# Kernel optimization log

Hardware: AMD Instinct MI355X
Metric: run time of the kernel (lower is better)

## Reference

```python
import jax, jax.numpy as jnp
import numpy as np

N_NODES = 50000
N_EDGES = 800000
F_IN, HID, N_CLS = 128, 64, 40
KS = 2  # kernel_size, dim=1, open B-spline, degree=1


def spline_conv(x, src, dst, pseudo, W, root, bias, num_nodes, kernel_size):
    """SplineConv (torch_geometric), dim=1, degree=1, open spline, aggr='mean'."""
    K = kernel_size
    v = pseudo[:, 0] * (K - 1)                       # map [0,1] -> [0, K-1]
    k0 = jnp.clip(jnp.floor(v), 0, K - 2)
    frac = v - k0                                    # linear (degree-1) basis
    i0 = k0.astype(jnp.int32)
    i1 = i0 + 1
    E = src.shape[0]
    e = jnp.arange(E)
    # per-edge kernel coefficients c[e,k] = sum_s basis[e,s]*[idx[e,s]==k]
    c = jnp.zeros((E, K), x.dtype).at[e, i0].add(1.0 - frac).at[e, i1].add(frac)
    xj = x[src]                                      # [E, F_in] gather
    # agg[k] = scatter-add over edges of c[e,k]*xj[e] -> [K, N, F_in]
    agg = jnp.stack([
        jax.ops.segment_sum(c[:, k:k + 1] * xj, dst, num_segments=num_nodes)
        for k in range(K)
    ])
    deg = jax.ops.segment_sum(jnp.ones((E,), x.dtype), dst, num_segments=num_nodes)
    msg = jnp.einsum('kni,kio->no', agg, W) / jnp.maximum(deg, 1.0)[:, None]
    return msg + x @ root + bias


def setup_inputs() -> dict:
    key = jax.random.key(0)
    ks = jax.random.split(key, 9)
    def glorot(k, shape):
        fan_in, fan_out = shape[-2], shape[-1]
        lim = (6.0 / (fan_in + fan_out)) ** 0.5
        return jax.random.uniform(k, shape, jnp.float32, -lim, lim)
    return {
        'x': jax.random.normal(ks[0], (N_NODES, F_IN), jnp.float32),
        'edge_index': jax.random.randint(ks[1], (2, N_EDGES), 0, N_NODES, jnp.int32),
        'edge_attr': jax.random.uniform(ks[2], (N_EDGES, 1), jnp.float32),
        'W1': glorot(ks[3], (KS, F_IN, HID)),
        'root1': glorot(ks[4], (F_IN, HID)),
        'bias1': jnp.zeros((HID,), jnp.float32),
        'W2': glorot(ks[5], (KS, HID, N_CLS)),
        'root2': glorot(ks[6], (HID, N_CLS)),
        'bias2': jnp.zeros((N_CLS,), jnp.float32),
    }


def reference(x, edge_index, edge_attr, W1, root1, bias1, W2, root2, bias2):
    src, dst = edge_index[0], edge_index[1]
    # eval mode: dropout is identity
    h = spline_conv(x, src, dst, edge_attr, W1, root1, bias1, N_NODES, KS)
    h = jax.nn.elu(h)
    out = spline_conv(h, src, dst, edge_attr, W2, root2, bias2, N_NODES, KS)
    return out
```

## Files before the change

### kernel.cpp

```cpp
#include <hip/hip_runtime.h>
#include <math.h>

#define N_NODES 50000
#define N_EDGES 800000
#define F_IN    128
#define HID     64
#define N_CLS   40

#define M1 (3 * HID)
#define K2  192
#define C2P 64

#define RANGE_SZ 6250
#define PERM_SLICES 128
#define PERM_CHUNK (N_EDGES / PERM_SLICES)
#define EST 64

#define NW (M1 * F_IN + C2P * K2)

using sh8 = __attribute__((ext_vector_type(8))) short;
using floatx4 = __attribute__((ext_vector_type(4))) float;

__device__ inline unsigned short f2bf(float f) {
    union { float f; unsigned int u; } c{f};
    unsigned int r = (c.u + 0x7FFF + ((c.u >> 16) & 1)) >> 16;
    return (unsigned short)r;
}
__device__ inline float bf2f(unsigned int u) {
    union { unsigned int u; float f; } c;
    c.u = u << 16;
    return c.f;
}

__global__ void concat_w(const float* __restrict__ W1, const float* __restrict__ root1,
                         const float* __restrict__ W2, const float* __restrict__ root2,
                         unsigned short* __restrict__ WT1, unsigned short* __restrict__ WT2,
                         int* __restrict__ cnt) {
    int i = blockIdx.x * blockDim.x + threadIdx.x;
    if (i < M1 * F_IN) {
        int c = i / F_IN, k = i % F_IN;
        float val;
        if (c < HID)            val = W1[k * HID + c];
        else if (c < 2 * HID)   val = W1[F_IN * HID + k * HID + (c - HID)];
        else                    val = root1[k * HID + (c - 2 * HID)];
        WT1[i] = f2bf(val);
    } else if (i < NW) {
        int ii = i - M1 * F_IN;
        int c = ii / K2, k = ii % K2;
        float val = 0.0f;
        if (c < N_CLS) {
            if (k < HID)             val = W2[k * N_CLS + c];
            else if (k < 2 * HID)    val = W2[HID * N_CLS + (k - HID) * N_CLS + c];
            else                     val = root2[(k - 2 * HID) * N_CLS + c];
        }
        WT2[ii] = f2bf(val);
    } else {
        int ii = i - NW;
        if (ii < N_NODES) cnt[ii] = 0;
    }
}

template <int KD, bool AF32, int SPLIT, int PW, int ROOTW, int MT>
__device__ __forceinline__ void gemm_body(int bid, const void* __restrict__ Aptr,
                                          const unsigned short* __restrict__ Bt,
                                          unsigned short* __restrict__ Csp,
                                          float* __restrict__ Croot, int Crows) {
    constexpr int KP = KD + 8;
    __shared__ unsigned short As[64 * KP];
    __shared__ unsigned short Bs[64 * KP];

    int tid = threadIdx.x;
    int row0 = bid * 64;

    if (AF32) {
        const float* A = (const float*)Aptr;
        for (int c = tid; c < 64 * (KD / 4); c += 256) {
            int r = c / (KD / 4), q = c % (KD / 4);
            int gr = row0 + r;
            float4 v = make_float4(0.f, 0.f, 0.f, 0.f);
            if (gr < Crows) v = *(const float4*)(A + (size_t)gr * KD + q * 4);
            union { unsigned short s[4]; uint2 u; } pk;
            pk.s[0] = f2bf(v.x); pk.s[1] = f2bf(v.y);
            pk.s[2] = f2bf(v.z); pk.s[3] = f2bf(v.w);
            *(uint2*)&As[r * KP + q * 4] = pk.u;
        }
    } else {
        const unsigned short* A = (const unsigned short*)Aptr;
        for (int c = tid; c < 64 * (KD / 8); c += 256) {
            int r = c / (KD / 8), q = c % (KD / 8);
            int gr = row0 + r;
            sh8 v = {};
            if (gr < Crows) v = *(const sh8*)(A + (size_t)gr * KD + q * 8);
            *(sh8*)&As[r * KP + q * 8] = v;
        }
    }

    int wv = tid >> 6, lane = tid & 63;
    int lrow = lane & 15, lq = lane >> 4;

    for (int mt = 0; mt < MT; ++mt) {
        int c0 = mt * 64;
        __syncthreads();
        for (int c = tid; c < 64 * (KD / 8); c += 256) {
            int r = c / (KD / 8), q = c % (KD / 8);
            *(sh8*)&Bs[r * KP + q * 8] = *(const sh8*)(Bt + (size_t)(c0 + r) * KD + q * 8);
        }
        __syncthreads();

        floatx4 acc[4] = {{0.f,0.f,0.f,0.f},{0.f,0.f,0.f,0.f},{0.f,0.f,0.f,0.f},{0.f,0.f,0.f,0.f}};
#pragma unroll
        for (int kt = 0; kt < KD / 32; ++kt) {
            int kb = kt * 32 + lq * 8;
            sh8 a0 = *(const sh8*)&As[(wv * 16 + lrow) * KP + kb];
#pragma unroll
            for (int cf = 0; cf < 4; ++cf) {
                sh8 b = *(const sh8*)&Bs[(cf * 16 + lrow) * KP + kb];
                acc[cf] = __builtin_amdgcn_mfma_f32_16x16x32_bf16(a0, b, acc[cf], 0, 0, 0);
            }
        }

#pragma unroll
        for (int r = 0; r < 4; ++r) {
            int gr = row0 + wv * 16 + lq * 4 + r;
            if (gr >= Crows) continue;
#pragma unroll
            for (int cf = 0; cf < 4; ++cf) {
                int gc = c0 + cf * 16 + lrow;
                float val = acc[cf][r];
                if (gc < SPLIT) {
                    int pi = (gc < PW) ? gc * 2 : (gc - PW) * 2 + 1;
                    Csp[(size_t)gr * SPLIT + pi] = f2bf(val);
                } else if (gc < SPLIT + ROOTW) {
                    Croot[(size_t)gr * ROOTW + (gc - SPLIT)] = val;
                }
            }
        }
    }
}

__device__ __forceinline__ void permute_body(int b, const int* __restrict__ src,
                                             const int* __restrict__ dst,
                                             const float* __restrict__ attr,
                                             int* __restrict__ cnt,
                                             unsigned int* __restrict__ edata) {
    int range = b & 7;
    int slice = b >> 3;
    int lo = range * RANGE_SZ;
    int e0 = slice * PERM_CHUNK;
    int e1 = e0 + PERM_CHUNK;
    for (int e = e0 + (int)threadIdx.x; e < e1; e += 256) {
        int d = dst[e];
        if ((unsigned)(d - lo) < (unsigned)RANGE_SZ) {
            int pos = atomicAdd(&cnt[d], 1);
            if (pos < EST) {
                unsigned int q = (unsigned int)(attr[e] * 65535.0f + 0.5f);
                edata[d * EST + pos] = (unsigned int)src[e] | (q << 16);
            }
        }
    }
}

__global__ __launch_bounds__(256) void gemm1_permute(const float* __restrict__ x,
                                                     const unsigned short* __restrict__ WT1,
                                                     unsigned short* __restrict__ Ysp,
                                                     float* __restrict__ Yroot,
                                                     const int* __restrict__ src,
                                                     const int* __restrict__ dst,
                                                     const float* __restrict__ attr,
                                                     int* __restrict__ cnt,
                                                     unsigned int* __restrict__ edata,
                                                     int gemmBlocks) {
    if ((int)blockIdx.x < gemmBlocks) {
        gemm_body<128, true, 128, 64, 64, 3>(blockIdx.x, (const void*)x, WT1, Ysp, Yroot, N_NODES);
    } else {
        permute_body(blockIdx.x - gemmBlocks, src, dst, attr, cnt, edata);
    }
}

__global__ __launch_bounds__(256) void gather1(const unsigned short* __restrict__ Ysp,
                                               const float* __restrict__ Yroot,
                                               const int* __restrict__ cnt,
                                               const unsigned int* __restrict__ edata,
                                               const float* __restrict__ bias1,
                                               unsigned short* __restrict__ h) {
    int wave = (blockIdx.x * blockDim.x + threadIdx.x) >> 6;
    int lane = threadIdx.x & 63;
    if (wave >= N_NODES) return;
    int hf = lane >> 5;
    int c  = lane & 31;
    int deg = cnt[wave];
    deg = deg > EST ? EST : deg;
    const unsigned int* eb = edata + (size_t)wave * EST;
    const float qs = 1.0f / 65535.0f;
    float a0 = 0.0f, a1 = 0.0f;
    if (deg <= 16) {
        unsigned int e[8]; uint2 p[8];
#pragma unroll
        for (int t = 0; t < 8; ++t) e[t] = eb[2 * t + hf];
#pragma unroll
        for (int t = 0; t < 8; ++t) {
            int idx = (2 * t + hf < deg) ? (int)(e[t] & 0xffffu) : 0;
            p[t] = *(const uint2*)(Ysp + (size_t)idx * 128 + c * 4);
        }
#pragma unroll
        for (int t = 0; t < 8; ++t) {
            float m = (2 * t + hf < deg) ? 1.0f : 0.0f;
            float v = (float)(e[t] >> 16) * qs;
            float w = 1.0f - v;
            a0 += m * (w * bf2f(p[t].x & 0xffffu) + v * bf2f(p[t].x >> 16));
            a1 += m * (w * bf2f(p[t].y & 0xffffu) + v * bf2f(p[t].y >> 16));
        }
    } else {
        unsigned int e[16]; uint2 p[16];
#pragma unroll
        for (int t = 0; t < 16; ++t) e[t] = eb[2 * t + hf];
#pragma unroll
        for (int t = 0; t < 16; ++t) {
            int idx = (2 * t + hf < deg) ? (int)(e[t] & 0xffffu) : 0;
            p[t] = *(const uint2*)(Ysp + (size_t)idx * 128 + c * 4);
        }
#pragma unroll
        for (int t = 0; t < 16; ++t) {
            float m = (2 * t + hf < deg) ? 1.0f : 0.0f;
            float v = (float)(e[t] >> 16) * qs;
            float w = 1.0f - v;
            a0 += m * (w * bf2f(p[t].x & 0xffffu) + v * bf2f(p[t].x >> 16));
            a1 += m * (w * bf2f(p[t].y & 0xffffu) + v * bf2f(p[t].y >> 16));
        }
        if (deg > 32) {
            for (int j = 32 + hf; j < deg; j += 2) {
                unsigned int ee = eb[j];
                int idx = (int)(ee & 0xffffu);
                uint2 pp = *(const uint2*)(Ysp + (size_t)idx * 128 + c * 4);
                float v = (float)(ee >> 16) * qs;
                float w = 1.0f - v;
                a0 += w * bf2f(pp.x & 0xffffu) + v * bf2f(pp.x >> 16);
                a1 += w * bf2f(pp.y & 0xffffu) + v * bf2f(pp.y >> 16);
            }
        }
    }
    a0 += __shfl_xor(a0, 32);
    a1 += __shfl_xor(a1, 32);
    float dg = (float)deg;
    dg = dg > 1.0f ? dg : 1.0f;
    float2 yr = *(const float2*)(Yroot + (size_t)wave * HID + c * 2);
    float2 bi = *(const float2*)(bias1 + c * 2);
    float m0 = a0 / dg + yr.x + bi.x;
    float m1 = a1 / dg + yr.y + bi.y;
    m0 = m0 > 0.0f ? m0 : expm1f(m0);
    m1 = m1 > 0.0f ? m1 : expm1f(m1);
    if (hf == 0) {
        unsigned int u = (unsigned int)f2bf(m0) | ((unsigned int)f2bf(m1) << 16);
        *(unsigned int*)(h + (size_t)wave * HID + c * 2) = u;
    }
}

__global__ __launch_bounds__(256) void g2gemm(const unsigned short* __restrict__ hb,
                                              const int* __restrict__ cnt,
                                              const unsigned int* __restrict__ edata,
                                              const unsigned short* __restrict__ WT2,
                                              const float* __restrict__ bias2,
                                              float* __restrict__ out) {
    constexpr int AP = 200;
    __shared__ unsigned short As[64 * AP];
    int tid = threadIdx.x;
    int row0 = blockIdx.x * 64;
    int wv = tid >> 6, lane = tid & 63;
    int hf = lane >> 5, c = lane & 31;
    const float qs = 1.0f / 65535.0f;

    for (int i = 0; i < 16; ++i) {
        int arow = wv * 16 + i;
        int node = row0 + arow;
        float a00 = 0.0f, a01 = 0.0f, a10 = 0.0f, a11 = 0.0f;
        int deg = 0;
        if (node < N_NODES) {
            deg = cnt[node];
            deg = deg > EST ? EST : deg;
            const unsigned int* eb = edata + (size_t)node * EST;
            if (deg <= 16) {
                unsigned int e[8], p[8];
#pragma unroll
                for (int t = 0; t < 8; ++t) e[t] = eb[2 * t + hf];
#pragma unroll
                for (int t = 0; t < 8; ++t) {
                    int idx = (2 * t + hf < deg) ? (int)(e[t] & 0xffffu) : 0;
                    p[t] = *(const unsigned int*)(hb + (size_t)idx * HID + c * 2);
                }
#pragma unroll
                for (int t = 0; t < 8; ++t) {
                    float m = (2 * t + hf < deg) ? 1.0f : 0.0f;
                    float v = (float)(e[t] >> 16) * qs;
                    float wm = m * (1.0f - v), vm = m * v;
                    float h0 = bf2f(p[t] & 0xffffu), h1 = bf2f(p[t] >> 16);
                    a00 += wm * h0; a01 += wm * h1;
                    a10 += vm * h0; a11 += vm * h1;
                }
            } else {
                unsigned int e[16], p[16];
#pragma unroll
                for (int t = 0; t < 16; ++t) e[t] = eb[2 * t + hf];
#pragma unroll
                for (int t = 0; t < 16; ++t) {
                    int idx = (2 * t + hf < deg) ? (int)(e[t] & 0xffffu) : 0;
                    p[t] = *(const unsigned int*)(hb + (size_t)idx * HID + c * 2);
                }
#pragma unroll
                for (int t = 0; t < 16; ++t) {
                    float m = (2 * t + hf < deg) ? 1.0f : 0.0f;
                    float v = (float)(e[t] >> 16) * qs;
                    float wm = m * (1.0f - v), vm = m * v;
                    float h0 = bf2f(p[t] & 0xffffu), h1 = bf2f(p[t] >> 16);
                    a00 += wm * h0; a01 += wm * h1;
                    a10 += vm * h0; a11 += vm * h1;
                }
                if (deg > 32) {
                    for (int j = 32 + hf; j < deg; j += 2) {
                        unsigned int ee = eb[j];
                        int idx = (int)(ee & 0xffffu);
                        unsigned int pp = *(const unsigned int*)(hb + (size_t)idx * HID + c * 2);
                        float v = (float)(ee >> 16) * qs;
                        float w = 1.0f - v;
                        float h0 = bf2f(pp & 0xffffu), h1 = bf2f(pp >> 16);
                        a00 += w * h0; a01 += w * h1;
                        a10 += v * h0; a11 += v * h1;
                    }
                }
            }
        }
        a00 += __shfl_xor(a00, 32);
        a01 += __shfl_xor(a01, 32);
        a10 += __shfl_xor(a10, 32);
        a11 += __shfl_xor(a11, 32);
        if (node < N_NODES) {
            if (hf == 0) {
                float dg = (float)deg;
                dg = dg > 1.0f ? dg : 1.0f;
                float inv = 1.0f / dg;
                unsigned int u0 = (unsigned int)f2bf(a00 * inv) | ((unsigned int)f2bf(a01 * inv) << 16);
                unsigned int u1 = (unsigned int)f2bf(a10 * inv) | ((unsigned int)f2bf(a11 * inv) << 16);
                *(unsigned int*)&As[arow * AP + c * 2] = u0;
                *(unsigned int*)&As[arow * AP + 64 + c * 2] = u1;
            } else {
                unsigned int u = *(const unsigned int*)(hb + (size_t)node * HID + c * 2);
                *(unsigned int*)&As[arow * AP + 128 + c * 2] = u;
            }
        } else {
            if (hf == 0) {
                *(unsigned int*)&As[arow * AP + c * 2] = 0u;
                *(unsigned int*)&As[arow * AP + 64 + c * 2] = 0u;
            } else {
                *(unsigned int*)&As[arow * AP + 128 + c * 2] = 0u;
            }
        }
    }
    __syncthreads();

    int lrow = lane & 15, lq = lane >> 4;
    floatx4 acc[4] = {{0.f,0.f,0.f,0.f},{0.f,0.f,0.f,0.f},{0.f,0.f,0.f,0.f},{0.f,0.f,0.f,0.f}};
#pragma unroll
    for (int kt = 0; kt < K2 / 32; ++kt) {
        int kb = kt * 32 + lq * 8;
        sh8 a0 = *(const sh8*)&As[(wv * 16 + lrow) * AP + kb];
#pragma unroll
        for (int cf = 0; cf < 4; ++cf) {
            sh8 b = *(const sh8*)(WT2 + (size_t)(cf * 16 + lrow) * K2 + kb);
            acc[cf] = __builtin_amdgcn_mfma_f32_16x16x32_bf16(a0, b, acc[cf], 0, 0, 0);
        }
    }

#pragma unroll
    for (int r = 0; r < 4; ++r) {
        int gr = row0 + wv * 16 + lq * 4 + r;
        if (gr >= N_NODES) continue;
#pragma unroll
        for (int cf = 0; cf < 4; ++cf) {
            int gc = cf * 16 + lrow;
            if (gc < N_CLS) {
                out[(size_t)gr * N_CLS + gc] = acc[cf][r] + bias2[gc];
            }
        }
    }
}

extern "C" void kernel_launch(void* const* d_in, const int* in_sizes, int n_in,
                              void* d_out, int out_size, void* d_ws, size_t ws_size,
                              hipStream_t stream) {
    const float* x     = (const float*)d_in[0];
    const int*   eidx  = (const int*)d_in[1];
    const float* eattr = (const float*)d_in[2];
    const float* W1    = (const float*)d_in[3];
    const float* root1 = (const float*)d_in[4];
    const float* bias1 = (const float*)d_in[5];
    const float* W2    = (const float*)d_in[6];
    const float* root2 = (const float*)d_in[7];
    const float* bias2 = (const float*)d_in[8];
    float* out = (float*)d_out;

    const int* src = eidx;
    const int* dst = eidx + N_EDGES;

    char* base = (char*)d_ws;
    unsigned short* Ysp   = (unsigned short*)base;
    float*          Yroot = (float*)(base + 12800000);
    unsigned short* hb    = (unsigned short*)(base + 25600000);
    unsigned short* WT1   = (unsigned short*)(base + 32000000);
    unsigned short* WT2   = (unsigned short*)(base + 32049152);
    unsigned int*   edata = (unsigned int*)(base + 32073728);
    int*            cnt   = (int*)(base + 44873728);

    const int GB = (N_NODES + 63) / 64;

    hipLaunchKernelGGL(concat_w, dim3((NW + N_NODES + 255) / 256), dim3(256), 0, stream,
                       W1, root1, W2, root2, WT1, WT2, cnt);

    hipLaunchKernelGGL(gemm1_permute, dim3(GB + 8 * PERM_SLICES), dim3(256), 0, stream,
                       x, WT1, Ysp, Yroot, src, dst, eattr, cnt, edata, GB);

    hipLaunchKernelGGL(gather1, dim3((N_NODES * 64 + 255) / 256), dim3(256), 0, stream,
                       Ysp, Yroot, cnt, edata, bias1, hb);

    hipLaunchKernelGGL(g2gemm, dim3(GB), dim3(256), 0, stream,
                       hb, cnt, edata, WT2, bias2, out);
}
```

Measured before the change: 209.2 us.

## Split edge permute into halves overlapped with GEMM and gather; separate layer-2 gather

```diff
diff --git a/kernel.cpp b/kernel.cpp
--- a/kernel.cpp
+++ b/kernel.cpp
@@ -11,9 +11,9 @@
 #define K2  192
 #define C2P 64
 
-#define RANGE_SZ 6250
-#define PERM_SLICES 128
-#define PERM_CHUNK (N_EDGES / PERM_SLICES)
+#define RHALF 25000
+#define PS2 256
+#define PCH (N_EDGES / PS2)
 #define EST 64
 
 #define NW (M1 * F_IN + C2P * K2)
@@ -138,51 +138,169 @@
     }
 }
 
-__device__ __forceinline__ void permute_body(int b, const int* __restrict__ src,
+__device__ __forceinline__ void permute_half(int slice, int lo,
+                                             const int* __restrict__ src,
                                              const int* __restrict__ dst,
                                              const float* __restrict__ attr,
                                              int* __restrict__ cnt,
                                              unsigned int* __restrict__ edata) {
-    int range = b & 7;
-    int slice = b >> 3;
-    int lo = range * RANGE_SZ;
-    int e0 = slice * PERM_CHUNK;
-    int e1 = e0 + PERM_CHUNK;
-    for (int e = e0 + (int)threadIdx.x; e < e1; e += 256) {
-        int d = dst[e];
-        if ((unsigned)(d - lo) < (unsigned)RANGE_SZ) {
-            int pos = atomicAdd(&cnt[d], 1);
-            if (pos < EST) {
+    int e0 = slice * PCH;
+    int e1 = e0 + PCH;
+    for (int base = e0 + (int)threadIdx.x; base < e1; base += 256 * 8) {
+        int d[8];
+        unsigned int pay[8];
+        int pos[8];
+#pragma unroll
+        for (int t = 0; t < 8; ++t) {
+            int e = base + t * 256;
+            d[t] = (e < e1) ? dst[e] : -1;
+        }
+#pragma unroll
+        for (int t = 0; t < 8; ++t) {
+            int e = base + t * 256;
+            pay[t] = 0u;
+            if ((unsigned)(d[t] - lo) < (unsigned)RHALF) {
                 unsigned int q = (unsigned int)(attr[e] * 65535.0f + 0.5f);
-                edata[d * EST + pos] = (unsigned int)src[e] | (q << 16);
-            }
-        }
-    }
-}
-
-__global__ __launch_bounds__(256) void gemm1_permute(const float* __restrict__ x,
-                                                     const unsigned short* __restrict__ WT1,
-                                                     unsigned short* __restrict__ Ysp,
-                                                     float* __restrict__ Yroot,
-                                                     const int* __restrict__ src,
-                                                     const int* __restrict__ dst,
-                                                     const float* __restrict__ attr,
-                                                     int* __restrict__ cnt,
-                                                     unsigned int* __restrict__ edata,
-                                                     int gemmBlocks) {
-    if ((int)blockIdx.x < gemmBlocks) {
-        gemm_body<128, true, 128, 64, 64, 3>(blockIdx.x, (const void*)x, WT1, Ysp, Yroot, N_NODES);
-    } else {
-        permute_body(blockIdx.x - gemmBlocks, src, dst, attr, cnt, edata);
-    }
-}
-
-__global__ __launch_bounds__(256) void gather1(const unsigned short* __restrict__ Ysp,
-                                               const float* __restrict__ Yroot,
-                                               const int* __restrict__ cnt,
-                                               const unsigned int* __restrict__ edata,
-                                               const float* __restrict__ bias1,
-                                               unsigned short* __restrict__ h) {
+                pay[t] = (unsigned int)src[e] | (q << 16);
+            }
+        }
+#pragma unroll
+        for (int t = 0; t < 8; ++t) {
+            pos[t] = ((unsigned)(d[t] - lo) < (unsigned)RHALF) ? atomicAdd(&cnt[d[t]], 1) : 0;
+        }
+#pragma unroll
+        for (int t = 0; t < 8; ++t) {
+            if ((unsigned)(d[t] - lo) < (unsigned)RHALF && pos[t] < EST)
+                edata[d[t] * EST + pos[t]] = pay[t];
+        }
+    }
+}
+
+__device__ __forceinline__ void gather1_body(int local_bid, int n0, int ncount,
+                                             const unsigned short* __restrict__ Ysp,
+                                             const float* __restrict__ Yroot,
+                                             const int* __restrict__ cnt,
+                                             const unsigned int* __restrict__ edata,
+                                             const float* __restrict__ bias1,
+                                             unsigned short* __restrict__ h) {
+    int wl = local_bid * 4 + ((int)threadIdx.x >> 6);
+    int lane = threadIdx.x & 63;
+    if (wl >= ncount) return;
+    int node = n0 + wl;
+    int hf = lane >> 5;
+    int c  = lane & 31;
+    int deg = cnt[node];
+    deg = deg > EST ? EST : deg;
+    const unsigned int* eb = edata + (size_t)node * EST;
+    const float qs = 1.0f / 65535.0f;
+    float a0 = 0.0f, a1 = 0.0f;
+    if (deg <= 16) {
+        unsigned int e[8]; uint2 p[8];
+#pragma unroll
+        for (int t = 0; t < 8; ++t) e[t] = eb[2 * t + hf];
+#pragma unroll
+        for (int t = 0; t < 8; ++t) {
+            int idx = (2 * t + hf < deg) ? (int)(e[t] & 0xffffu) : 0;
+            p[t] = *(const uint2*)(Ysp + (size_t)idx * 128 + c * 4);
+        }
+#pragma unroll
+        for (int t = 0; t < 8; ++t) {
+            float m = (2 * t + hf < deg) ? 1.0f : 0.0f;
+            float v = (float)(e[t] >> 16) * qs;
+            float w = 1.0f - v;
+            a0 += m * (w * bf2f(p[t].x & 0xffffu) + v * bf2f(p[t].x >> 16));
+            a1 += m * (w * bf2f(p[t].y & 0xffffu) + v * bf2f(p[t].y >> 16));
+        }
+    } else {
+        unsigned int e[16]; uint2 p[16];
+#pragma unroll
+        for (int t = 0; t < 16; ++t) e[t] = eb[2 * t + hf];
+#pragma unroll
+        for (int t = 0; t < 16; ++t) {
+            int idx = (2 * t + hf < deg) ? (int)(e[t] & 0xffffu) : 0;
+            p[t] = *(const uint2*)(Ysp + (size_t)idx * 128 + c * 4);
+        }
+#pragma unroll
+        for (int t = 0; t < 16; ++t) {
+            float m = (2 * t + hf < deg) ? 1.0f : 0.0f;
+            float v = (float)(e[t] >> 16) * qs;
+            float w = 1.0f - v;
+            a0 += m * (w * bf2f(p[t].x & 0xffffu) + v * bf2f(p[t].x >> 16));
+            a1 += m * (w * bf2f(p[t].y & 0xffffu) + v * bf2f(p[t].y >> 16));
+        }
+        if (deg > 32) {
+            for (int j = 32 + hf; j < deg; j += 2) {
+                unsigned int ee = eb[j];
+                int idx = (int)(ee & 0xffffu);
+                uint2 pp = *(const uint2*)(Ysp + (size_t)idx * 128 + c * 4);
+                float v = (float)(ee >> 16) * qs;
+                float w = 1.0f - v;
+                a0 += w * bf2f(pp.x & 0xffffu) + v * bf2f(pp.x >> 16);
+                a1 += w * bf2f(pp.y & 0xffffu) + v * bf2f(pp.y >> 16);
+            }
+        }
+    }
+    a0 += __shfl_xor(a0, 32);
+    a1 += __shfl_xor(a1, 32);
+    float dg = (float)deg;
+    dg = dg > 1.0f ? dg : 1.0f;
+    float2 yr = *(const float2*)(Yroot + (size_t)node * HID + c * 2);
+    float2 bi = *(const float2*)(bias1 + c * 2);
+    float m0 = a0 / dg + yr.x + bi.x;
+    float m1 = a1 / dg + yr.y + bi.y;
+    m0 = m0 > 0.0f ? m0 : expm1f(m0);
+    m1 = m1 > 0.0f ? m1 : expm1f(m1);
+    if (hf == 0) {
+        unsigned int u = (unsigned int)f2bf(m0) | ((unsigned int)f2bf(m1) << 16);
+        *(unsigned int*)(h + (size_t)node * HID + c * 2) = u;
+    }
+}
+
+__global__ __launch_bounds__(256) void gemm1_permA(const float* __restrict__ x,
+                                                   const unsigned short* __restrict__ WT1,
+                                                   unsigned short* __restrict__ Ysp,
+                                                   float* __restrict__ Yroot,
+                                                   const int* __restrict__ src,
+                                                   const int* __restrict__ dst,
+                                                   const float* __restrict__ attr,
+                                                   int* __restrict__ cnt,
+                                                   unsigned int* __restrict__ edata) {
+    if ((int)blockIdx.x < PS2) {
+        permute_half(blockIdx.x, 0, src, dst, attr, cnt, edata);
+    } else {
+        gemm_body<128, true, 128, 64, 64, 3>(blockIdx.x - PS2, (const void*)x, WT1, Ysp, Yroot, N_NODES);
+    }
+}
+
+__global__ __launch_bounds__(256) void permB_g1A(const unsigned short* __restrict__ Ysp,
+                                                 const float* __restrict__ Yroot,
+                                                 int* __restrict__ cnt,
+                                                 unsigned int* __restrict__ edata,
+                                                 const float* __restrict__ bias1,
+                                                 unsigned short* __restrict__ hb,
+                                                 const int* __restrict__ src,
+                                                 const int* __restrict__ dst,
+                                                 const float* __restrict__ attr) {
+    if ((int)blockIdx.x < PS2) {
+        permute_half(blockIdx.x, RHALF, src, dst, attr, cnt, edata);
+    } else {
+        gather1_body(blockIdx.x - PS2, 0, RHALF, Ysp, Yroot, cnt, edata, bias1, hb);
+    }
+}
+
+__global__ __launch_bounds__(256) void g1B(const unsigned short* __restrict__ Ysp,
+                                           const float* __restrict__ Yroot,
+                                           const int* __restrict__ cnt,
+                                           const unsigned int* __restrict__ edata,
+                                           const float* __restrict__ bias1,
+                                           unsigned short* __restrict__ hb) {
+    gather1_body(blockIdx.x, RHALF, N_NODES - RHALF, Ysp, Yroot, cnt, edata, bias1, hb);
+}
+
+__global__ __launch_bounds__(256) void gather2h(const unsigned short* __restrict__ hb,
+                                                const int* __restrict__ cnt,
+                                                const unsigned int* __restrict__ edata,
+                                                unsigned short* __restrict__ A128) {
     int wave = (blockIdx.x * blockDim.x + threadIdx.x) >> 6;
     int lane = threadIdx.x & 63;
     if (wave >= N_NODES) return;
@@ -192,183 +310,106 @@
     deg = deg > EST ? EST : deg;
     const unsigned int* eb = edata + (size_t)wave * EST;
     const float qs = 1.0f / 65535.0f;
-    float a0 = 0.0f, a1 = 0.0f;
+    float a00 = 0.0f, a01 = 0.0f, a10 = 0.0f, a11 = 0.0f;
     if (deg <= 16) {
-        unsigned int e[8]; uint2 p[8];
+        unsigned int e[8], p[8];
 #pragma unroll
         for (int t = 0; t < 8; ++t) e[t] = eb[2 * t + hf];
 #pragma unroll
         for (int t = 0; t < 8; ++t) {
             int idx = (2 * t + hf < deg) ? (int)(e[t] & 0xffffu) : 0;
-            p[t] = *(const uint2*)(Ysp + (size_t)idx * 128 + c * 4);
+            p[t] = *(const unsigned int*)(hb + (size_t)idx * HID + c * 2);
         }
 #pragma unroll
         for (int t = 0; t < 8; ++t) {
             float m = (2 * t + hf < deg) ? 1.0f : 0.0f;
             float v = (float)(e[t] >> 16) * qs;
-            float w = 1.0f - v;
-            a0 += m * (w * bf2f(p[t].x & 0xffffu) + v * bf2f(p[t].x >> 16));
-            a1 += m * (w * bf2f(p[t].y & 0xffffu) + v * bf2f(p[t].y >> 16));
-        }
-    } else {
-        unsigned int e[16]; uint2 p[16];
+            float wm = m * (1.0f - v), vm = m * v;
+            float h0 = bf2f(p[t] & 0xffffu), h1 = bf2f(p[t] >> 16);
+            a00 += wm * h0; a01 += wm * h1;
+            a10 += vm * h0; a11 += vm * h1;
+        }
+    } else {
+        unsigned int e[16], p[16];
 #pragma unroll
         for (int t = 0; t < 16; ++t) e[t] = eb[2 * t + hf];
 #pragma unroll
         for (int t = 0; t < 16; ++t) {
             int idx = (2 * t + hf < deg) ? (int)(e[t] & 0xffffu) : 0;
-            p[t] = *(const uint2*)(Ysp + (size_t)idx * 128 + c * 4);
+            p[t] = *(const unsigned int*)(hb + (size_t)idx * HID + c * 2);
         }
 #pragma unroll
         for (int t = 0; t < 16; ++t) {
             float m = (2 * t + hf < deg) ? 1.0f : 0.0f;
             float v = (float)(e[t] >> 16) * qs;
-            float w = 1.0f - v;
-            a0 += m * (w * bf2f(p[t].x & 0xffffu) + v * bf2f(p[t].x >> 16));
-            a1 += m * (w * bf2f(p[t].y & 0xffffu) + v * bf2f(p[t].y >> 16));
+            float wm = m * (1.0f - v), vm = m * v;
+            float h0 = bf2f(p[t] & 0xffffu), h1 = bf2f(p[t] >> 16);
+            a00 += wm * h0; a01 += wm * h1;
+            a10 += vm * h0; a11 += vm * h1;
         }
         if (deg > 32) {
             for (int j = 32 + hf; j < deg; j += 2) {
                 unsigned int ee = eb[j];
                 int idx = (int)(ee & 0xffffu);
-                uint2 pp = *(const uint2*)(Ysp + (size_t)idx * 128 + c * 4);
+                unsigned int pp = *(const unsigned int*)(hb + (size_t)idx * HID + c * 2);
                 float v = (float)(ee >> 16) * qs;
                 float w = 1.0f - v;
-                a0 += w * bf2f(pp.x & 0xffffu) + v * bf2f(pp.x >> 16);
-                a1 += w * bf2f(pp.y & 0xffffu) + v * bf2f(pp.y >> 16);
-            }
-        }
-    }
-    a0 += __shfl_xor(a0, 32);
-    a1 += __shfl_xor(a1, 32);
-    float dg = (float)deg;
-    dg = dg > 1.0f ? dg : 1.0f;
-    float2 yr = *(const float2*)(Yroot + (size_t)wave * HID + c * 2);
-    float2 bi = *(const float2*)(bias1 + c * 2);
-    float m0 = a0 / dg + yr.x + bi.x;
-    float m1 = a1 / dg + yr.y + bi.y;
-    m0 = m0 > 0.0f ? m0 : expm1f(m0);
-    m1 = m1 > 0.0f ? m1 : expm1f(m1);
+                float h0 = bf2f(pp & 0xffffu), h1 = bf2f(pp >> 16);
+                a00 += w * h0; a01 += w * h1;
+                a10 += v * h0; a11 += v * h1;
+            }
+        }
+    }
+    a00 += __shfl_xor(a00, 32);
+    a01 += __shfl_xor(a01, 32);
+    a10 += __shfl_xor(a10, 32);
+    a11 += __shfl_xor(a11, 32);
     if (hf == 0) {
-        unsigned int u = (unsigned int)f2bf(m0) | ((unsigned int)f2bf(m1) << 16);
-        *(unsigned int*)(h + (size_t)wave * HID + c * 2) = u;
-    }
-}
-
-__global__ __launch_bounds__(256) void g2gemm(const unsigned short* __restrict__ hb,
-                                              const int* __restrict__ cnt,
-                                              const unsigned int* __restrict__ edata,
-                                              const unsigned short* __restrict__ WT2,
-                                              const float* __restrict__ bias2,
-                                              float* __restrict__ out) {
-    constexpr int AP = 200;
-    __shared__ unsigned short As[64 * AP];
+        float dg = (float)deg;
+        dg = dg > 1.0f ? dg : 1.0f;
+        float inv = 1.0f / dg;
+        unsigned int u0 = (unsigned int)f2bf(a00 * inv) | ((unsigned int)f2bf(a01 * inv) << 16);
+        unsigned int u1 = (unsigned int)f2bf(a10 * inv) | ((unsigned int)f2bf(a11 * inv) << 16);
+        *(unsigned int*)(A128 + (size_t)wave * 128 + c * 2) = u0;
+        *(unsigned int*)(A128 + (size_t)wave * 128 + 64 + c * 2) = u1;
+    }
+}
+
+__global__ __launch_bounds__(256) void gemm_out(const unsigned short* __restrict__ A128,
+                                                const unsigned short* __restrict__ hb,
+                                                const unsigned short* __restrict__ WT2,
+                                                const float* __restrict__ bias2,
+                                                float* __restrict__ out) {
+    constexpr int KD = K2, KP = KD + 8;
+    __shared__ unsigned short As[64 * KP];
     int tid = threadIdx.x;
     int row0 = blockIdx.x * 64;
+
+    for (int cidx = tid; cidx < 64 * (KD / 8); cidx += 256) {
+        int r = cidx / (KD / 8), q = cidx % (KD / 8);
+        int gr = row0 + r;
+        sh8 v = {};
+        if (gr < N_NODES) {
+            if (q < 16) v = *(const sh8*)(A128 + (size_t)gr * 128 + q * 8);
+            else        v = *(const sh8*)(hb + (size_t)gr * 64 + (q - 16) * 8);
+        }
+        *(sh8*)&As[r * KP + q * 8] = v;
+    }
+    __syncthreads();
+
     int wv = tid >> 6, lane = tid & 63;
-    int hf = lane >> 5, c = lane & 31;
-    const float qs = 1.0f / 65535.0f;
-
-    for (int i = 0; i < 16; ++i) {
-        int arow = wv * 16 + i;
-        int node = row0 + arow;
-        float a00 = 0.0f, a01 = 0.0f, a10 = 0.0f, a11 = 0.0f;
-        int deg = 0;
-        if (node < N_NODES) {
-            deg = cnt[node];
-            deg = deg > EST ? EST : deg;
-            const unsigned int* eb = edata + (size_t)node * EST;
-            if (deg <= 16) {
-                unsigned int e[8], p[8];
-#pragma unroll
-                for (int t = 0; t < 8; ++t) e[t] = eb[2 * t + hf];
-#pragma unroll
-                for (int t = 0; t < 8; ++t) {
-                    int idx = (2 * t + hf < deg) ? (int)(e[t] & 0xffffu) : 0;
-                    p[t] = *(const unsigned int*)(hb + (size_t)idx * HID + c * 2);
-                }
-#pragma unroll
-                for (int t = 0; t < 8; ++t) {
-                    float m = (2 * t + hf < deg) ? 1.0f : 0.0f;
-                    float v = (float)(e[t] >> 16) * qs;
-                    float wm = m * (1.0f - v), vm = m * v;
-                    float h0 = bf2f(p[t] & 0xffffu), h1 = bf2f(p[t] >> 16);
-                    a00 += wm * h0; a01 += wm * h1;
-                    a10 += vm * h0; a11 += vm * h1;
-                }
-            } else {
-                unsigned int e[16], p[16];
-#pragma unroll
-                for (int t = 0; t < 16; ++t) e[t] = eb[2 * t + hf];
-#pragma unroll
-                for (int t = 0; t < 16; ++t) {
-                    int idx = (2 * t + hf < deg) ? (int)(e[t] & 0xffffu) : 0;
-                    p[t] = *(const unsigned int*)(hb + (size_t)idx * HID + c * 2);
-                }
-#pragma unroll
-                for (int t = 0; t < 16; ++t) {
-                    float m = (2 * t + hf < deg) ? 1.0f : 0.0f;
-                    float v = (float)(e[t] >> 16) * qs;
-                    float wm = m * (1.0f - v), vm = m * v;
-                    float h0 = bf2f(p[t] & 0xffffu), h1 = bf2f(p[t] >> 16);
-                    a00 += wm * h0; a01 += wm * h1;
-                    a10 += vm * h0; a11 += vm * h1;
-                }
-                if (deg > 32) {
-                    for (int j = 32 + hf; j < deg; j += 2) {
-                        unsigned int ee = eb[j];
-                        int idx = (int)(ee & 0xffffu);
-                        unsigned int pp = *(const unsigned int*)(hb + (size_t)idx * HID + c * 2);
-                        float v = (float)(ee >> 16) * qs;
-                        float w = 1.0f - v;
-                        float h0 = bf2f(pp & 0xffffu), h1 = bf2f(pp >> 16);
-                        a00 += w * h0; a01 += w * h1;
-                        a10 += v * h0; a11 += v * h1;
-                    }
-                }
-            }
-        }
-        a00 += __shfl_xor(a00, 32);
-        a01 += __shfl_xor(a01, 32);
-        a10 += __shfl_xor(a10, 32);
-        a11 += __shfl_xor(a11, 32);
-        if (node < N_NODES) {
-            if (hf == 0) {
-                float dg = (float)deg;
-                dg = dg > 1.0f ? dg : 1.0f;
-                float inv = 1.0f / dg;
-                unsigned int u0 = (unsigned int)f2bf(a00 * inv) | ((unsigned int)f2bf(a01 * inv) << 16);
-                unsigned int u1 = (unsigned int)f2bf(a10 * inv) | ((unsigned int)f2bf(a11 * inv) << 16);
-                *(unsigned int*)&As[arow * AP + c * 2] = u0;
-                *(unsigned int*)&As[arow * AP + 64 + c * 2] = u1;
-            } else {
-                unsigned int u = *(const unsigned int*)(hb + (size_t)node * HID + c * 2);
-                *(unsigned int*)&As[arow * AP + 128 + c * 2] = u;
-            }
-        } else {
-            if (hf == 0) {
-                *(unsigned int*)&As[arow * AP + c * 2] = 0u;
-                *(unsigned int*)&As[arow * AP + 64 + c * 2] = 0u;
-            } else {
-                *(unsigned int*)&As[arow * AP + 128 + c * 2] = 0u;
-            }
-        }
-    }
-    __syncthreads();
-
     int lrow = lane & 15, lq = lane >> 4;
     floatx4 acc[4] = {{0.f,0.f,0.f,0.f},{0.f,0.f,0.f,0.f},{0.f,0.f,0.f,0.f},{0.f,0.f,0.f,0.f}};
 #pragma unroll
-    for (int kt = 0; kt < K2 / 32; ++kt) {
+    for (int kt = 0; kt < KD / 32; ++kt) {
         int kb = kt * 32 + lq * 8;
-        sh8 a0 = *(const sh8*)&As[(wv * 16 + lrow) * AP + kb];
+        sh8 a0 = *(const sh8*)&As[(wv * 16 + lrow) * KP + kb];
 #pragma unroll
         for (int cf = 0; cf < 4; ++cf) {
-            sh8 b = *(const sh8*)(WT2 + (size_t)(cf * 16 + lrow) * K2 + kb);
+            sh8 b = *(const sh8*)(WT2 + (size_t)(cf * 16 + lrow) * KD + kb);
             acc[cf] = __builtin_amdgcn_mfma_f32_16x16x32_bf16(a0, b, acc[cf], 0, 0, 0);
         }
     }
-
 #pragma unroll
     for (int r = 0; r < 4; ++r) {
         int gr = row0 + wv * 16 + lq * 4 + r;
@@ -408,18 +449,25 @@
     unsigned short* WT2   = (unsigned short*)(base + 32049152);
     unsigned int*   edata = (unsigned int*)(base + 32073728);
     int*            cnt   = (int*)(base + 44873728);
+    unsigned short* A128  = (unsigned short*)(base + 45073728);
 
     const int GB = (N_NODES + 63) / 64;
 
     hipLaunchKernelGGL(concat_w, dim3((NW + N_NODES + 255) / 256), dim3(256), 0, stream,
                        W1, root1, W2, root2, WT1, WT2, cnt);
 
-    hipLaunchKernelGGL(gemm1_permute, dim3(GB + 8 * PERM_SLICES), dim3(256), 0, stream,
-                       x, WT1, Ysp, Yroot, src, dst, eattr, cnt, edata, GB);
-
-    hipLaunchKernelGGL(gather1, dim3((N_NODES * 64 + 255) / 256), dim3(256), 0, stream,
+    hipLaunchKernelGGL(gemm1_permA, dim3(PS2 + GB), dim3(256), 0, stream,
+                       x, WT1, Ysp, Yroot, src, dst, eattr, cnt, edata);
+
+    hipLaunchKernelGGL(permB_g1A, dim3(PS2 + RHALF / 4), dim3(256), 0, stream,
+                       Ysp, Yroot, cnt, edata, bias1, hb, src, dst, eattr);
+
+    hipLaunchKernelGGL(g1B, dim3((N_NODES - RHALF) / 4), dim3(256), 0, stream,
                        Ysp, Yroot, cnt, edata, bias1, hb);
 
-    hipLaunchKernelGGL(g2gemm, dim3(GB), dim3(256), 0, stream,
-                       hb, cnt, edata, WT2, bias2, out);
-}
+    hipLaunchKernelGGL(gather2h, dim3((N_NODES * 64 + 255) / 256), dim3(256), 0, stream,
+                       hb, cnt, edata, A128);
+
+    hipLaunchKernelGGL(gemm_out, dim3(GB), dim3(256), 0, stream,
+                       A128, hb, WT2, bias2, out);
+}
```

After: 206.2 us. No clear change (-1.5%).

## Split layer-2 gather from GEMM and overlap halves across staged kernels

Applied to the files above, without the earlier changes.

```diff
diff --git a/kernel.cpp b/kernel.cpp
--- a/kernel.cpp
+++ b/kernel.cpp
@@ -15,6 +15,12 @@
 #define PERM_SLICES 128
 #define PERM_CHUNK (N_EDGES / PERM_SLICES)
 #define EST 64
+
+#define RSPLIT 25024
+#define GA_BLK (RSPLIT / 64)
+#define GB2_BLK ((N_NODES - RSPLIT + 63) / 64)
+#define G2A_BLK (RSPLIT / 4)
+#define G2B_BLK ((N_NODES - RSPLIT + 3) / 4)
 
 #define NW (M1 * F_IN + C2P * K2)
 
@@ -255,120 +261,122 @@
     }
 }
 
-__global__ __launch_bounds__(256) void g2gemm(const unsigned short* __restrict__ hb,
+__device__ __forceinline__ void gather2h_body(int local_bid, int n0, int ncount,
+                                              const unsigned short* __restrict__ hb,
                                               const int* __restrict__ cnt,
                                               const unsigned int* __restrict__ edata,
+                                              unsigned short* __restrict__ A128) {
+    int wl = local_bid * 4 + ((int)threadIdx.x >> 6);
+    int lane = threadIdx.x & 63;
+    if (wl >= ncount) return;
+    int node = n0 + wl;
+    int hf = lane >> 5;
+    int c  = lane & 31;
+    int deg = cnt[node];
+    deg = deg > EST ? EST : deg;
+    const unsigned int* eb = edata + (size_t)node * EST;
+    const float qs = 1.0f / 65535.0f;
+    float a00 = 0.0f, a01 = 0.0f, a10 = 0.0f, a11 = 0.0f;
+    if (deg <= 16) {
+        unsigned int e[8], p[8];
+#pragma unroll
+        for (int t = 0; t < 8; ++t) e[t] = eb[2 * t + hf];
+#pragma unroll
+        for (int t = 0; t < 8; ++t) {
+            int idx = (2 * t + hf < deg) ? (int)(e[t] & 0xffffu) : 0;
+            p[t] = *(const unsigned int*)(hb + (size_t)idx * HID + c * 2);
+        }
+#pragma unroll
+        for (int t = 0; t < 8; ++t) {
+            float m = (2 * t + hf < deg) ? 1.0f : 0.0f;
+            float v = (float)(e[t] >> 16) * qs;
+            float wm = m * (1.0f - v), vm = m * v;
+            float h0 = bf2f(p[t] & 0xffffu), h1 = bf2f(p[t] >> 16);
+            a00 += wm * h0; a01 += wm * h1;
+            a10 += vm * h0; a11 += vm * h1;
+        }
+    } else {
+        unsigned int e[16], p[16];
+#pragma unroll
+        for (int t = 0; t < 16; ++t) e[t] = eb[2 * t + hf];
+#pragma unroll
+        for (int t = 0; t < 16; ++t) {
+            int idx = (2 * t + hf < deg) ? (int)(e[t] & 0xffffu) : 0;
+            p[t] = *(const unsigned int*)(hb + (size_t)idx * HID + c * 2);
+        }
+#pragma unroll
+        for (int t = 0; t < 16; ++t) {
+            float m = (2 * t + hf < deg) ? 1.0f : 0.0f;
+            float v = (float)(e[t] >> 16) * qs;
+            float wm = m * (1.0f - v), vm = m * v;
+            float h0 = bf2f(p[t] & 0xffffu), h1 = bf2f(p[t] >> 16);
+            a00 += wm * h0; a01 += wm * h1;
+            a10 += vm * h0; a11 += vm * h1;
+        }
+        if (deg > 32) {
+            for (int j = 32 + hf; j < deg; j += 2) {
+                unsigned int ee = eb[j];
+                int idx = (int)(ee & 0xffffu);
+                unsigned int pp = *(const unsigned int*)(hb + (size_t)idx * HID + c * 2);
+                float v = (float)(ee >> 16) * qs;
+                float w = 1.0f - v;
+                float h0 = bf2f(pp & 0xffffu), h1 = bf2f(pp >> 16);
+                a00 += w * h0; a01 += w * h1;
+                a10 += v * h0; a11 += v * h1;
+            }
+        }
+    }
+    a00 += __shfl_xor(a00, 32);
+    a01 += __shfl_xor(a01, 32);
+    a10 += __shfl_xor(a10, 32);
+    a11 += __shfl_xor(a11, 32);
+    if (hf == 0) {
+        float dg = (float)deg;
+        dg = dg > 1.0f ? dg : 1.0f;
+        float inv = 1.0f / dg;
+        unsigned int u0 = (unsigned int)f2bf(a00 * inv) | ((unsigned int)f2bf(a01 * inv) << 16);
+        unsigned int u1 = (unsigned int)f2bf(a10 * inv) | ((unsigned int)f2bf(a11 * inv) << 16);
+        *(unsigned int*)(A128 + (size_t)node * 128 + c * 2) = u0;
+        *(unsigned int*)(A128 + (size_t)node * 128 + 64 + c * 2) = u1;
+    }
+}
+
+__device__ __forceinline__ void gemm_out_body(int bid, int rowbase,
+                                              const unsigned short* __restrict__ A128,
+                                              const unsigned short* __restrict__ hb,
                                               const unsigned short* __restrict__ WT2,
                                               const float* __restrict__ bias2,
                                               float* __restrict__ out) {
-    constexpr int AP = 200;
-    __shared__ unsigned short As[64 * AP];
+    constexpr int KD = K2, KP = KD + 8;
+    __shared__ unsigned short As[64 * KP];
     int tid = threadIdx.x;
-    int row0 = blockIdx.x * 64;
+    int row0 = rowbase + bid * 64;
+
+    for (int cidx = tid; cidx < 64 * (KD / 8); cidx += 256) {
+        int r = cidx / (KD / 8), q = cidx % (KD / 8);
+        int gr = row0 + r;
+        sh8 v = {};
+        if (gr < N_NODES) {
+            if (q < 16) v = *(const sh8*)(A128 + (size_t)gr * 128 + q * 8);
+            else        v = *(const sh8*)(hb + (size_t)gr * 64 + (q - 16) * 8);
+        }
+        *(sh8*)&As[r * KP + q * 8] = v;
+    }
+    __syncthreads();
+
     int wv = tid >> 6, lane = tid & 63;
-    int hf = lane >> 5, c = lane & 31;
-    const float qs = 1.0f / 65535.0f;
-
-    for (int i = 0; i < 16; ++i) {
-        int arow = wv * 16 + i;
-        int node = row0 + arow;
-        float a00 = 0.0f, a01 = 0.0f, a10 = 0.0f, a11 = 0.0f;
-        int deg = 0;
-        if (node < N_NODES) {
-            deg = cnt[node];
-            deg = deg > EST ? EST : deg;
-            const unsigned int* eb = edata + (size_t)node * EST;
-            if (deg <= 16) {
-                unsigned int e[8], p[8];
-#pragma unroll
-                for (int t = 0; t < 8; ++t) e[t] = eb[2 * t + hf];
-#pragma unroll
-                for (int t = 0; t < 8; ++t) {
-                    int idx = (2 * t + hf < deg) ? (int)(e[t] & 0xffffu) : 0;
-                    p[t] = *(const unsigned int*)(hb + (size_t)idx * HID + c * 2);
-                }
-#pragma unroll
-                for (int t = 0; t < 8; ++t) {
-                    float m = (2 * t + hf < deg) ? 1.0f : 0.0f;
-                    float v = (float)(e[t] >> 16) * qs;
-                    float wm = m * (1.0f - v), vm = m * v;
-                    float h0 = bf2f(p[t] & 0xffffu), h1 = bf2f(p[t] >> 16);
-                    a00 += wm * h0; a01 += wm * h1;
-                    a10 += vm * h0; a11 += vm * h1;
-                }
-            } else {
-                unsigned int e[16], p[16];
-#pragma unroll
-                for (int t = 0; t < 16; ++t) e[t] = eb[2 * t + hf];
-#pragma unroll
-                for (int t = 0; t < 16; ++t) {
-                    int idx = (2 * t + hf < deg) ? (int)(e[t] & 0xffffu) : 0;
-                    p[t] = *(const unsigned int*)(hb + (size_t)idx * HID + c * 2);
-                }
-#pragma unroll
-                for (int t = 0; t < 16; ++t) {
-                    float m = (2 * t + hf < deg) ? 1.0f : 0.0f;
-                    float v = (float)(e[t] >> 16) * qs;
-                    float wm = m * (1.0f - v), vm = m * v;
-                    float h0 = bf2f(p[t] & 0xffffu), h1 = bf2f(p[t] >> 16);
-                    a00 += wm * h0; a01 += wm * h1;
-                    a10 += vm * h0; a11 += vm * h1;
-                }
-                if (deg > 32) {
-                    for (int j = 32 + hf; j < deg; j += 2) {
-                        unsigned int ee = eb[j];
-                        int idx = (int)(ee & 0xffffu);
-                        unsigned int pp = *(const unsigned int*)(hb + (size_t)idx * HID + c * 2);
-                        float v = (float)(ee >> 16) * qs;
-                        float w = 1.0f - v;
-                        float h0 = bf2f(pp & 0xffffu), h1 = bf2f(pp >> 16);
-                        a00 += w * h0; a01 += w * h1;
-                        a10 += v * h0; a11 += v * h1;
-                    }
-                }
-            }
-        }
-        a00 += __shfl_xor(a00, 32);
-        a01 += __shfl_xor(a01, 32);
-        a10 += __shfl_xor(a10, 32);
-        a11 += __shfl_xor(a11, 32);
-        if (node < N_NODES) {
-            if (hf == 0) {
-                float dg = (float)deg;
-                dg = dg > 1.0f ? dg : 1.0f;
-                float inv = 1.0f / dg;
-                unsigned int u0 = (unsigned int)f2bf(a00 * inv) | ((unsigned int)f2bf(a01 * inv) << 16);
-                unsigned int u1 = (unsigned int)f2bf(a10 * inv) | ((unsigned int)f2bf(a11 * inv) << 16);
-                *(unsigned int*)&As[arow * AP + c * 2] = u0;
-                *(unsigned int*)&As[arow * AP + 64 + c * 2] = u1;
-            } else {
-                unsigned int u = *(const unsigned int*)(hb + (size_t)node * HID + c * 2);
-                *(unsigned int*)&As[arow * AP + 128 + c * 2] = u;
-            }
-        } else {
-            if (hf == 0) {
-                *(unsigned int*)&As[arow * AP + c * 2] = 0u;
-                *(unsigned int*)&As[arow * AP + 64 + c * 2] = 0u;
-            } else {
-                *(unsigned int*)&As[arow * AP + 128 + c * 2] = 0u;
-            }
-        }
-    }
-    __syncthreads();
-
     int lrow = lane & 15, lq = lane >> 4;
     floatx4 acc[4] = {{0.f,0.f,0.f,0.f},{0.f,0.f,0.f,0.f},{0.f,0.f,0.f,0.f},{0.f,0.f,0.f,0.f}};
 #pragma unroll
-    for (int kt = 0; kt < K2 / 32; ++kt) {
+    for (int kt = 0; kt < KD / 32; ++kt) {
         int kb = kt * 32 + lq * 8;
-        sh8 a0 = *(const sh8*)&As[(wv * 16 + lrow) * AP + kb];
+        sh8 a0 = *(const sh8*)&As[(wv * 16 + lrow) * KP + kb];
 #pragma unroll
         for (int cf = 0; cf < 4; ++cf) {
-            sh8 b = *(const sh8*)(WT2 + (size_t)(cf * 16 + lrow) * K2 + kb);
+            sh8 b = *(const sh8*)(WT2 + (size_t)(cf * 16 + lrow) * KD + kb);
             acc[cf] = __builtin_amdgcn_mfma_f32_16x16x32_bf16(a0, b, acc[cf], 0, 0, 0);
         }
     }
-
 #pragma unroll
     for (int r = 0; r < 4; ++r) {
         int gr = row0 + wv * 16 + lq * 4 + r;
@@ -381,6 +389,35 @@
             }
         }
     }
+}
+
+__global__ __launch_bounds__(256) void g2hA(const unsigned short* __restrict__ hb,
+                                            const int* __restrict__ cnt,
+                                            const unsigned int* __restrict__ edata,
+                                            unsigned short* __restrict__ A128) {
+    gather2h_body(blockIdx.x, 0, RSPLIT, hb, cnt, edata, A128);
+}
+
+__global__ __launch_bounds__(256) void g2hB_outA(const unsigned short* __restrict__ hb,
+                                                 const int* __restrict__ cnt,
+                                                 const unsigned int* __restrict__ edata,
+                                                 unsigned short* __restrict__ A128,
+                                                 const unsigned short* __restrict__ WT2,
+                                                 const float* __restrict__ bias2,
+                                                 float* __restrict__ out) {
+    if ((int)blockIdx.x < G2B_BLK) {
+        gather2h_body(blockIdx.x, RSPLIT, N_NODES - RSPLIT, hb, cnt, edata, A128);
+    } else {
+        gemm_out_body(blockIdx.x - G2B_BLK, 0, A128, hb, WT2, bias2, out);
+    }
+}
+
+__global__ __launch_bounds__(256) void outB(const unsigned short* __restrict__ A128,
+                                            const unsigned short* __restrict__ hb,
+                                            const unsigned short* __restrict__ WT2,
+                                            const float* __restrict__ bias2,
+                                            float* __restrict__ out) {
+    gemm_out_body(blockIdx.x, RSPLIT, A128, hb, WT2, bias2, out);
 }
 
 extern "C" void kernel_launch(void* const* d_in, const int* in_sizes, int n_in,
@@ -408,6 +445,7 @@
     unsigned short* WT2   = (unsigned short*)(base + 32049152);
     unsigned int*   edata = (unsigned int*)(base + 32073728);
     int*            cnt   = (int*)(base + 44873728);
+    unsigned short* A128  = (unsigned short*)(base + 45073728);
 
     const int GB = (N_NODES + 63) / 64;
 
@@ -420,6 +458,12 @@
     hipLaunchKernelGGL(gather1, dim3((N_NODES * 64 + 255) / 256), dim3(256), 0, stream,
                        Ysp, Yroot, cnt, edata, bias1, hb);
 
-    hipLaunchKernelGGL(g2gemm, dim3(GB), dim3(256), 0, stream,
-                       hb, cnt, edata, WT2, bias2, out);
-}
+    hipLaunchKernelGGL(g2hA, dim3(G2A_BLK), dim3(256), 0, stream,
+                       hb, cnt, edata, A128);
+
+    hipLaunchKernelGGL(g2hB_outA, dim3(G2B_BLK + GA_BLK), dim3(256), 0, stream,
+                       hb, cnt, edata, A128, WT2, bias2, out);
+
+    hipLaunchKernelGGL(outB, dim3(GB2_BLK), dim3(256), 0, stream,
+                       A128, hb, WT2, bias2, out);
+}
```

Result: no change. 209.3 us (+0.0%).
